# Kernel optimization log

Measured on AMD Instinct MI355X. Metric: run time of the kernel, lower is better.

Reference implementation:

```python
import jax, jax.numpy as jnp
import numpy as np

T, H, D = 8192, 2048, 1024

def setup_inputs() -> dict:
    key = jax.random.key(0)
    k1, k2, k3 = jax.random.split(key, 3)
    x_sequence = jax.random.normal(k1, (T, D), dtype=jnp.float32)
    lamda = jax.random.normal(k2, (H,), dtype=jnp.float32) * 0.2
    B = jax.random.normal(k3, (H, D), dtype=jnp.float32) / jnp.sqrt(jnp.float32(D))
    return {"x_sequence": x_sequence, "lamda": lamda, "B": B}

def reference(x_sequence, lamda, B):
    # Batch all input projections into one GEMM: u[t] = B @ x[t]  -> [T, H]
    u = jnp.einsum('td,hd->th', x_sequence, B)
    a = jax.nn.sigmoid(lamda)  # [H], time-invariant diagonal decay

    def step(h, u_t):
        h = a * h + u_t
        return h, h

    h0 = jnp.zeros_like(lamda)
    _, outputs = jax.lax.scan(step, h0, u)  # [T, H]
    return outputs
```

## Files before the change

kernel.cpp:

```cpp
#include <hip/hip_runtime.h>
#include <hip/hip_bf16.h>

#define T_DIM 8192
#define H_DIM 2048
#define D_DIM 1024
#define PAD_R 32
#define MT    160
#define NT    128
#define BK    64
#define USTR  128

typedef __bf16 bf16x8 __attribute__((ext_vector_type(8)));
typedef float floatx4 __attribute__((ext_vector_type(4)));
typedef unsigned short u16;

__device__ __forceinline__ u16 f2bf(float f) {
    __hip_bfloat16 b = __float2bfloat16(f);
    return *reinterpret_cast<u16*>(&b);
}
__device__ __forceinline__ float bf2f(u16 v) {
    return __uint_as_float((unsigned)v << 16);
}

__global__ __launch_bounds__(256) void conv_kernel(const float* __restrict__ x,
                                                   const float* __restrict__ Bm,
                                                   u16* __restrict__ xb,
                                                   u16* __restrict__ bb) {
    const int nPad4 = PAD_R * D_DIM / 4;
    const int nX4   = (T_DIM + PAD_R) * D_DIM / 4;
    const int nB4   = H_DIM * D_DIM / 4;
    int i = blockIdx.x * 256 + threadIdx.x;
    if (i < nX4) {
        ushort4 o;
        if (i < nPad4) {
            o.x = o.y = o.z = o.w = 0;
        } else {
            const float4 v = reinterpret_cast<const float4*>(x)[i - nPad4];
            o.x = f2bf(v.x); o.y = f2bf(v.y); o.z = f2bf(v.z); o.w = f2bf(v.w);
        }
        reinterpret_cast<ushort4*>(xb)[i] = o;
    } else {
        i -= nX4;
        if (i >= nB4) return;
        const float4 v = reinterpret_cast<const float4*>(Bm)[i];
        ushort4 o;
        o.x = f2bf(v.x); o.y = f2bf(v.y); o.z = f2bf(v.z); o.w = f2bf(v.w);
        reinterpret_cast<ushort4*>(bb)[i] = o;
    }
}

#define GLDS(g, l) \
    __builtin_amdgcn_global_load_lds((const __attribute__((address_space(1))) void*)(g), \
                                     (__attribute__((address_space(3))) void*)(l), 16, 0, 0)

__global__ __launch_bounds__(256) void fused_kernel(const u16* __restrict__ xb,
                                                    const u16* __restrict__ bb,
                                                    const float* __restrict__ lam,
                                                    float* __restrict__ out) {
    __shared__ alignas(16) u16 smem[MT * USTR];
    u16* sA = smem;
    u16* sB = smem + MT * BK;
    u16* us = smem;

    const int tid  = threadIdx.x;
    const int lane = tid & 63;
    const int wid  = tid >> 6;
    const int pm0  = blockIdx.y * 128;
    const int n0   = blockIdx.x * 128;
    const int wm   = (wid >> 1) * 80;
    const int wn   = (wid & 1) * 64;
    const int lrow = lane & 15;
    const int kseg = lane >> 4;

    floatx4 acc[5][4] = {};

    const int r_s = tid >> 3;
    const int cg  = ((tid & 7) * 8) ^ ((r_s & 7) * 8);

    const u16* gA = xb + (size_t)(pm0 + r_s) * D_DIM + cg;
    const u16* gB = bb + (size_t)(n0 + r_s) * D_DIM + cg;

    const bf16x8* pA = reinterpret_cast<const bf16x8*>(sA);
    const bf16x8* pB = reinterpret_cast<const bf16x8*>(sB);

    for (int it = 0; it < D_DIM / BK; ++it) {
#pragma unroll
        for (int q = 0; q < 5; ++q)
            GLDS(gA + (size_t)(q * 32) * D_DIM, &sA[q * 2048 + tid * 8]);
#pragma unroll
        for (int q = 0; q < 4; ++q)
            GLDS(gB + (size_t)(q * 32) * D_DIM, &sB[q * 2048 + tid * 8]);
        gA += BK; gB += BK;
        __syncthreads();

#pragma unroll
        for (int kk = 0; kk < BK; kk += 32) {
            bf16x8 af[5], bf[4];
#pragma unroll
            for (int i = 0; i < 5; ++i) {
                const int row = wm + i * 16 + lrow;
                const int cp  = (kk + kseg * 8) ^ ((row & 7) * 8);
                af[i] = pA[(row * BK + cp) >> 3];
            }
#pragma unroll
            for (int j = 0; j < 4; ++j) {
                const int row = wn + j * 16 + lrow;
                const int cp  = (kk + kseg * 8) ^ ((row & 7) * 8);
                bf[j] = pB[(row * BK + cp) >> 3];
            }
#pragma unroll
            for (int i = 0; i < 5; ++i)
#pragma unroll
                for (int j = 0; j < 4; ++j)
                    acc[i][j] = __builtin_amdgcn_mfma_f32_16x16x32_bf16(af[i], bf[j], acc[i][j], 0, 0, 0);
        }
        __syncthreads();
    }

#pragma unroll
    for (int i = 0; i < 5; ++i) {
#pragma unroll
        for (int j = 0; j < 4; ++j) {
            const int col = wn + j * 16 + lrow;
#pragma unroll
            for (int r = 0; r < 4; ++r) {
                const int row = wm + i * 16 + kseg * 4 + r;
                us[row * USTR + (col ^ (kseg * 16))] = f2bf(acc[i][j][r]);
            }
        }
    }
    __syncthreads();

    {
        const int half = tid >> 7;
        const int c    = tid & 127;
        const float a  = 1.0f / (1.0f + __expf(-lam[n0 + c]));
        float hs = 0.0f;
        const int rbase = half * 64;
        float* op = out + (size_t)(blockIdx.y * 128 + half * 64) * H_DIM + (n0 + c);
#pragma unroll 8
        for (int q = 0; q < 32; ++q) {
            const int tl = rbase + q;
            hs = fmaf(a, hs, bf2f(us[tl * USTR + (c ^ (((tl >> 2) & 3) * 16))]));
        }
#pragma unroll 8
        for (int q = 0; q < 64; ++q) {
            const int tl = rbase + 32 + q;
            hs = fmaf(a, hs, bf2f(us[tl * USTR + (c ^ (((tl >> 2) & 3) * 16))]));
            op[(size_t)q * H_DIM] = hs;
        }
    }
}

extern "C" void kernel_launch(void* const* d_in, const int* in_sizes, int n_in,
                              void* d_out, int out_size, void* d_ws, size_t ws_size,
                              hipStream_t stream) {
    const float* x   = (const float*)d_in[0];
    const float* lam = (const float*)d_in[1];
    const float* B   = (const float*)d_in[2];
    float* out = (float*)d_out;

    u16* xb = (u16*)d_ws;
    u16* bb = xb + (size_t)(T_DIM + PAD_R) * D_DIM;

    const int n4 = ((T_DIM + PAD_R) * D_DIM + H_DIM * D_DIM) / 4;
    conv_kernel<<<(n4 + 255) / 256, 256, 0, stream>>>(x, B, xb, bb);
    fused_kernel<<<dim3(H_DIM / 128, T_DIM / 128), 256, 0, stream>>>(xb, bb, lam, out);
}
```

Baseline: 148.1 us.

## Split fused GEMM+scan into pipelined 256x256 GEMM and separate scan kernel

Replaces the fused GEMM-plus-local-scan kernel, which used 160-row tiles overlapping into previous rows, with a 256x256-tile GEMM. The new GEMM uses 512 threads, double-buffered global-to-LDS loads, barrier-staged MFMA quads with priority hints and XCD-aware block mapping, and writes bf16 u to workspace. A separate scan kernel then rescans with a 32-step warmup and two channels per thread. The aim is to remove the redundant A-tile recompute and raise MFMA efficiency. The cost is an extra bf16 round trip of u through global memory and one more launch.

```diff
diff --git a/kernel.cpp b/kernel.cpp
--- a/kernel.cpp
+++ b/kernel.cpp
@@ -4,11 +4,7 @@
 #define T_DIM 8192
 #define H_DIM 2048
 #define D_DIM 1024
-#define PAD_R 32
-#define MT    160
-#define NT    128
-#define BK    64
-#define USTR  128
+#define KT    16
 
 typedef __bf16 bf16x8 __attribute__((ext_vector_type(8)));
 typedef float floatx4 __attribute__((ext_vector_type(4)));
@@ -21,134 +17,217 @@
 __device__ __forceinline__ float bf2f(u16 v) {
     return __uint_as_float((unsigned)v << 16);
 }
+
+#define GLDS(g, l) \
+    __builtin_amdgcn_global_load_lds((const __attribute__((address_space(1))) void*)(g), \
+                                     (__attribute__((address_space(3))) void*)(l), 16, 0, 0)
 
 __global__ __launch_bounds__(256) void conv_kernel(const float* __restrict__ x,
                                                    const float* __restrict__ Bm,
                                                    u16* __restrict__ xb,
                                                    u16* __restrict__ bb) {
-    const int nPad4 = PAD_R * D_DIM / 4;
-    const int nX4   = (T_DIM + PAD_R) * D_DIM / 4;
-    const int nB4   = H_DIM * D_DIM / 4;
+    const int nX4 = T_DIM * D_DIM / 4;
+    const int nB4 = H_DIM * D_DIM / 4;
     int i = blockIdx.x * 256 + threadIdx.x;
+    const float4* src;
+    ushort4* dst;
     if (i < nX4) {
-        ushort4 o;
-        if (i < nPad4) {
-            o.x = o.y = o.z = o.w = 0;
-        } else {
-            const float4 v = reinterpret_cast<const float4*>(x)[i - nPad4];
-            o.x = f2bf(v.x); o.y = f2bf(v.y); o.z = f2bf(v.z); o.w = f2bf(v.w);
-        }
-        reinterpret_cast<ushort4*>(xb)[i] = o;
+        src = reinterpret_cast<const float4*>(x) + i;
+        dst = reinterpret_cast<ushort4*>(xb) + i;
     } else {
         i -= nX4;
         if (i >= nB4) return;
-        const float4 v = reinterpret_cast<const float4*>(Bm)[i];
-        ushort4 o;
-        o.x = f2bf(v.x); o.y = f2bf(v.y); o.z = f2bf(v.z); o.w = f2bf(v.w);
-        reinterpret_cast<ushort4*>(bb)[i] = o;
-    }
-}
-
-#define GLDS(g, l) \
-    __builtin_amdgcn_global_load_lds((const __attribute__((address_space(1))) void*)(g), \
-                                     (__attribute__((address_space(3))) void*)(l), 16, 0, 0)
-
-__global__ __launch_bounds__(256) void fused_kernel(const u16* __restrict__ xb,
-                                                    const u16* __restrict__ bb,
-                                                    const float* __restrict__ lam,
-                                                    float* __restrict__ out) {
-    __shared__ alignas(16) u16 smem[MT * USTR];
+        src = reinterpret_cast<const float4*>(Bm) + i;
+        dst = reinterpret_cast<ushort4*>(bb) + i;
+    }
+    const float4 v = *src;
+    ushort4 o;
+    o.x = f2bf(v.x); o.y = f2bf(v.y); o.z = f2bf(v.z); o.w = f2bf(v.w);
+    *dst = o;
+}
+
+__device__ __forceinline__ bf16x8 lds_frag(const u16* base, int row, int kx, int kseg) {
+    const int cp = (kx + kseg * 8) ^ ((row & 7) * 8);
+    return *reinterpret_cast<const bf16x8*>(base + row * 64 + cp);
+}
+
+#define MFMA_QUAD(MH, NH, BF)                                                        \
+    _Pragma("unroll")                                                                \
+    for (int kx = 0; kx < 2; ++kx)                                                   \
+        _Pragma("unroll")                                                            \
+        for (int mi = 0; mi < 4; ++mi)                                               \
+            _Pragma("unroll")                                                        \
+            for (int nj = 0; nj < 2; ++nj)                                           \
+                acc[(MH) * 4 + mi][(NH) * 2 + nj] =                                  \
+                    __builtin_amdgcn_mfma_f32_16x16x32_bf16(                         \
+                        af[mi][kx], BF[nj][kx], acc[(MH) * 4 + mi][(NH) * 2 + nj],   \
+                        0, 0, 0);
+
+__global__ __launch_bounds__(512, 2) void gemm_kernel(const u16* __restrict__ xb,
+                                                      const u16* __restrict__ bb,
+                                                      u16* __restrict__ ub) {
+    __shared__ alignas(16) u16 smem[65536];
     u16* sA = smem;
-    u16* sB = smem + MT * BK;
-    u16* us = smem;
+    u16* sB = smem + 32768;
 
     const int tid  = threadIdx.x;
     const int lane = tid & 63;
     const int wid  = tid >> 6;
-    const int pm0  = blockIdx.y * 128;
-    const int n0   = blockIdx.x * 128;
-    const int wm   = (wid >> 1) * 80;
-    const int wn   = (wid & 1) * 64;
     const int lrow = lane & 15;
     const int kseg = lane >> 4;
-
-    floatx4 acc[5][4] = {};
-
-    const int r_s = tid >> 3;
-    const int cg  = ((tid & 7) * 8) ^ ((r_s & 7) * 8);
-
-    const u16* gA = xb + (size_t)(pm0 + r_s) * D_DIM + cg;
-    const u16* gB = bb + (size_t)(n0 + r_s) * D_DIM + cg;
-
-    const bf16x8* pA = reinterpret_cast<const bf16x8*>(sA);
-    const bf16x8* pB = reinterpret_cast<const bf16x8*>(sB);
-
-    for (int it = 0; it < D_DIM / BK; ++it) {
-#pragma unroll
-        for (int q = 0; q < 5; ++q)
-            GLDS(gA + (size_t)(q * 32) * D_DIM, &sA[q * 2048 + tid * 8]);
-#pragma unroll
-        for (int q = 0; q < 4; ++q)
-            GLDS(gB + (size_t)(q * 32) * D_DIM, &sB[q * 2048 + tid * 8]);
-        gA += BK; gB += BK;
-        __syncthreads();
-
-#pragma unroll
-        for (int kk = 0; kk < BK; kk += 32) {
-            bf16x8 af[5], bf[4];
-#pragma unroll
-            for (int i = 0; i < 5; ++i) {
-                const int row = wm + i * 16 + lrow;
-                const int cp  = (kk + kseg * 8) ^ ((row & 7) * 8);
-                af[i] = pA[(row * BK + cp) >> 3];
+    const int wm   = (wid >> 2) * 128;
+    const int wn   = (wid & 3) * 64;
+
+    const int bid = blockIdx.x;
+    const int xcd = bid & 7, idx = bid >> 3;
+    const int bn  = (xcd & 1) * 4 + (idx & 3);
+    const int bm  = (xcd >> 1) * 8 + (idx >> 2);
+
+    const int rS = tid >> 3;
+    const int cS = ((tid & 7) * 8) ^ ((rS & 7) * 8);
+    const u16* gA = xb + (size_t)(bm * 256 + rS) * D_DIM + cS;
+    const u16* gB = bb + (size_t)(bn * 256 + rS) * D_DIM + cS;
+
+    floatx4 acc[8][4] = {};
+    bf16x8 af[4][2], b0[2][2], b1[2][2];
+
+#pragma unroll
+    for (int hq = 0; hq < 4; ++hq)
+        GLDS(gA + (size_t)(hq * 64) * D_DIM, sA + hq * 4096 + tid * 8);
+#pragma unroll
+    for (int hq = 0; hq < 4; ++hq)
+        GLDS(gB + (size_t)(hq * 64) * D_DIM, sB + hq * 4096 + tid * 8);
+#pragma unroll
+    for (int hq = 0; hq < 4; ++hq)
+        GLDS(gB + (size_t)(hq * 64) * D_DIM + 64, sB + 16384 + hq * 4096 + tid * 8);
+    asm volatile("s_waitcnt vmcnt(4)" ::: "memory");
+    __builtin_amdgcn_s_barrier();
+
+#pragma unroll 2
+    for (int j = 0; j < KT; ++j) {
+        const u16* cA = sA + (j & 1) * 16384;
+        const u16* cB = sB + (j & 1) * 16384;
+        u16* dB       = sB + (j & 1) * 16384;
+        const u16* gb2 = gB + (size_t)(j + 2) * 64;
+
+#pragma unroll
+        for (int mi = 0; mi < 4; ++mi)
+#pragma unroll
+            for (int kx = 0; kx < 2; ++kx)
+                af[mi][kx] = lds_frag(cA, wm + mi * 16 + lrow, kx * 32, kseg);
+#pragma unroll
+        for (int nj = 0; nj < 2; ++nj)
+#pragma unroll
+            for (int kx = 0; kx < 2; ++kx)
+                b0[nj][kx] = lds_frag(cB, wn + nj * 16 + lrow, kx * 32, kseg);
+        if (j + 1 < KT) {
+            u16* dA = sA + ((j + 1) & 1) * 16384;
+            const u16* ga = gA + (size_t)(j + 1) * 64;
+#pragma unroll
+            for (int hq = 0; hq < 4; ++hq)
+                GLDS(ga + (size_t)(hq * 64) * D_DIM, dA + hq * 4096 + tid * 8);
+        }
+        __builtin_amdgcn_s_barrier();
+        asm volatile("s_waitcnt lgkmcnt(0)" ::: "memory");
+        __builtin_amdgcn_s_setprio(1);
+        MFMA_QUAD(0, 0, b0)
+        __builtin_amdgcn_s_setprio(0);
+        __builtin_amdgcn_s_barrier();
+
+#pragma unroll
+        for (int nj = 0; nj < 2; ++nj)
+#pragma unroll
+            for (int kx = 0; kx < 2; ++kx)
+                b1[nj][kx] = lds_frag(cB, wn + 32 + nj * 16 + lrow, kx * 32, kseg);
+        __builtin_amdgcn_s_barrier();
+        asm volatile("s_waitcnt lgkmcnt(0)" ::: "memory");
+        __builtin_amdgcn_s_setprio(1);
+        MFMA_QUAD(0, 1, b1)
+        __builtin_amdgcn_s_setprio(0);
+        __builtin_amdgcn_s_barrier();
+
+#pragma unroll
+        for (int mi = 0; mi < 4; ++mi)
+#pragma unroll
+            for (int kx = 0; kx < 2; ++kx)
+                af[mi][kx] = lds_frag(cA, wm + 64 + mi * 16 + lrow, kx * 32, kseg);
+        if (j + 2 < KT) {
+            GLDS(gb2, dB + tid * 8);
+            GLDS(gb2 + (size_t)64 * D_DIM, dB + 4096 + tid * 8);
+        }
+        __builtin_amdgcn_s_barrier();
+        asm volatile("s_waitcnt lgkmcnt(0)" ::: "memory");
+        __builtin_amdgcn_s_setprio(1);
+        MFMA_QUAD(1, 0, b0)
+        __builtin_amdgcn_s_setprio(0);
+        __builtin_amdgcn_s_barrier();
+
+        if (j + 2 < KT) {
+            GLDS(gb2 + (size_t)128 * D_DIM, dB + 8192 + tid * 8);
+            GLDS(gb2 + (size_t)192 * D_DIM, dB + 12288 + tid * 8);
+        }
+        __builtin_amdgcn_s_barrier();
+        asm volatile("s_waitcnt lgkmcnt(0)" ::: "memory");
+        __builtin_amdgcn_s_setprio(1);
+        MFMA_QUAD(1, 1, b1)
+        __builtin_amdgcn_s_setprio(0);
+        if (j < KT - 2) asm volatile("s_waitcnt vmcnt(4)" ::: "memory");
+        else            asm volatile("s_waitcnt vmcnt(0)" ::: "memory");
+        __builtin_amdgcn_s_barrier();
+    }
+
+    u16* ut = smem;
+#pragma unroll
+    for (int mi = 0; mi < 8; ++mi)
+#pragma unroll
+        for (int nj = 0; nj < 4; ++nj) {
+            const int col = wn + nj * 16 + lrow;
+#pragma unroll
+            for (int r = 0; r < 4; ++r) {
+                const int row = wm + mi * 16 + kseg * 4 + r;
+                ut[row * 256 + (col ^ (kseg * 16))] = f2bf(acc[mi][nj][r]);
             }
-#pragma unroll
-            for (int j = 0; j < 4; ++j) {
-                const int row = wn + j * 16 + lrow;
-                const int cp  = (kk + kseg * 8) ^ ((row & 7) * 8);
-                bf[j] = pB[(row * BK + cp) >> 3];
-            }
-#pragma unroll
-            for (int i = 0; i < 5; ++i)
-#pragma unroll
-                for (int j = 0; j < 4; ++j)
-                    acc[i][j] = __builtin_amdgcn_mfma_f32_16x16x32_bf16(af[i], bf[j], acc[i][j], 0, 0, 0);
-        }
-        __syncthreads();
-    }
-
-#pragma unroll
-    for (int i = 0; i < 5; ++i) {
-#pragma unroll
-        for (int j = 0; j < 4; ++j) {
-            const int col = wn + j * 16 + lrow;
-#pragma unroll
-            for (int r = 0; r < 4; ++r) {
-                const int row = wm + i * 16 + kseg * 4 + r;
-                us[row * USTR + (col ^ (kseg * 16))] = f2bf(acc[i][j][r]);
-            }
-        }
-    }
+        }
     __syncthreads();
-
     {
-        const int half = tid >> 7;
-        const int c    = tid & 127;
-        const float a  = 1.0f / (1.0f + __expf(-lam[n0 + c]));
-        float hs = 0.0f;
-        const int rbase = half * 64;
-        float* op = out + (size_t)(blockIdx.y * 128 + half * 64) * H_DIM + (n0 + c);
+        const int rr = tid >> 5, cc = tid & 31;
+#pragma unroll
+        for (int w = 0; w < 16; ++w) {
+            const int row = w * 16 + rr;
+            const int s = (row >> 2) & 3;
+            bf16x8 v = *reinterpret_cast<const bf16x8*>(&ut[row * 256 + ((cc * 8) ^ (s * 16))]);
+            *reinterpret_cast<bf16x8*>(&ub[(size_t)(bm * 256 + row) * H_DIM + bn * 256 + cc * 8]) = v;
+        }
+    }
+}
+
+__global__ __launch_bounds__(256) void scan_kernel(const u16* __restrict__ u,
+                                                   const float* __restrict__ lam,
+                                                   float* __restrict__ out) {
+    const int tid  = threadIdx.x;
+    const int half = tid >> 7;
+    const int c2   = (blockIdx.x * 128 + (tid & 127)) * 2;
+    const int t0   = blockIdx.y * 256 + half * 128;
+    const float a0 = 1.0f / (1.0f + __expf(-lam[c2]));
+    const float a1 = 1.0f / (1.0f + __expf(-lam[c2 + 1]));
+    float h0 = 0.0f, h1 = 0.0f;
+    const u16* up = u + (size_t)t0 * H_DIM + c2;
+    if (t0) {
+        const u16* uw = up - (size_t)32 * H_DIM;
 #pragma unroll 8
         for (int q = 0; q < 32; ++q) {
-            const int tl = rbase + q;
-            hs = fmaf(a, hs, bf2f(us[tl * USTR + (c ^ (((tl >> 2) & 3) * 16))]));
-        }
+            const unsigned v = *reinterpret_cast<const unsigned*>(uw + (size_t)q * H_DIM);
+            h0 = fmaf(a0, h0, bf2f((u16)v));
+            h1 = fmaf(a1, h1, bf2f((u16)(v >> 16)));
+        }
+    }
+    float2* op = reinterpret_cast<float2*>(out + (size_t)t0 * H_DIM + c2);
 #pragma unroll 8
-        for (int q = 0; q < 64; ++q) {
-            const int tl = rbase + 32 + q;
-            hs = fmaf(a, hs, bf2f(us[tl * USTR + (c ^ (((tl >> 2) & 3) * 16))]));
-            op[(size_t)q * H_DIM] = hs;
-        }
+    for (int q = 0; q < 128; ++q) {
+        const unsigned v = *reinterpret_cast<const unsigned*>(up + (size_t)q * H_DIM);
+        h0 = fmaf(a0, h0, bf2f((u16)v));
+        h1 = fmaf(a1, h1, bf2f((u16)(v >> 16)));
+        op[(size_t)q * (H_DIM / 2)] = make_float2(h0, h1);
     }
 }
 
@@ -161,9 +240,11 @@
     float* out = (float*)d_out;
 
     u16* xb = (u16*)d_ws;
-    u16* bb = xb + (size_t)(T_DIM + PAD_R) * D_DIM;
-
-    const int n4 = ((T_DIM + PAD_R) * D_DIM + H_DIM * D_DIM) / 4;
+    u16* bb = xb + (size_t)T_DIM * D_DIM;
+    u16* ub = bb + (size_t)H_DIM * D_DIM;
+
+    const int n4 = (T_DIM * D_DIM + H_DIM * D_DIM) / 4;
     conv_kernel<<<(n4 + 255) / 256, 256, 0, stream>>>(x, B, xb, bb);
-    fused_kernel<<<dim3(H_DIM / 128, T_DIM / 128), 256, 0, stream>>>(xb, bb, lam, out);
-}
+    gemm_kernel<<<256, 512, 0, stream>>>(xb, bb, ub);
+    scan_kernel<<<dim3(H_DIM / 256, T_DIM / 256), 256, 0, stream>>>(ub, lam, out);
+}
```

After: 144.7 us. 1.02x faster.

## Software-pipeline GEMM with double/triple-buffered LDS and XCD-aware block mapping

Applied to the files above, without the earlier changes.

Replaces the single-buffered K loop (BK=64, load-then-sync) with a BK=32 pipeline. A is double-buffered and B triple-buffered, with async global-to-LDS loads issued for future tiles while MFMAs run on the current one, using explicit vmcnt waits and setprio. The grid is flattened and block IDs remapped so each XCD handles a contiguous band of M rows, which should improve L2 reuse. LDS per block shrinks to about 44KB and launch bounds request 3 blocks per CU, trading register headroom for occupancy.

```diff
diff --git a/kernel.cpp b/kernel.cpp
--- a/kernel.cpp
+++ b/kernel.cpp
@@ -5,10 +5,7 @@
 #define H_DIM 2048
 #define D_DIM 1024
 #define PAD_R 32
-#define MT    160
-#define NT    128
-#define BK    64
-#define USTR  128
+#define KT2   32
 
 typedef __bf16 bf16x8 __attribute__((ext_vector_type(8)));
 typedef float floatx4 __attribute__((ext_vector_type(4)));
@@ -21,6 +18,10 @@
 __device__ __forceinline__ float bf2f(u16 v) {
     return __uint_as_float((unsigned)v << 16);
 }
+
+#define GLDS(g, l) \
+    __builtin_amdgcn_global_load_lds((const __attribute__((address_space(1))) void*)(g), \
+                                     (__attribute__((address_space(3))) void*)(l), 16, 0, 0)
 
 __global__ __launch_bounds__(256) void conv_kernel(const float* __restrict__ x,
                                                    const float* __restrict__ Bm,
@@ -49,105 +50,134 @@
     }
 }
 
-#define GLDS(g, l) \
-    __builtin_amdgcn_global_load_lds((const __attribute__((address_space(1))) void*)(g), \
-                                     (__attribute__((address_space(3))) void*)(l), 16, 0, 0)
+__device__ __forceinline__ bf16x8 lds_frag32(const u16* base, int row, int kseg) {
+    const int g = (kseg ^ ((row >> 1) & 3)) * 8;
+    return *reinterpret_cast<const bf16x8*>(base + row * 32 + g);
+}
 
-__global__ __launch_bounds__(256) void fused_kernel(const u16* __restrict__ xb,
-                                                    const u16* __restrict__ bb,
-                                                    const float* __restrict__ lam,
-                                                    float* __restrict__ out) {
-    __shared__ alignas(16) u16 smem[MT * USTR];
+#define PH_BAR()    __builtin_amdgcn_s_barrier()
+#define SCHEDB()    __builtin_amdgcn_sched_barrier(0)
+#define LGKM0()     do { asm volatile("s_waitcnt lgkmcnt(0)" ::: "memory"); \
+                         SCHEDB(); } while (0)
+
+__global__ __launch_bounds__(256, 3) void gemm_kernel(const u16* __restrict__ xb,
+                                                      const u16* __restrict__ bb,
+                                                      const float* __restrict__ lam,
+                                                      float* __restrict__ out) {
+    __shared__ alignas(16) u16 smem[22528];
     u16* sA = smem;
-    u16* sB = smem + MT * BK;
-    u16* us = smem;
+    u16* sB = smem + 10240;
 
     const int tid  = threadIdx.x;
     const int lane = tid & 63;
     const int wid  = tid >> 6;
-    const int pm0  = blockIdx.y * 128;
-    const int n0   = blockIdx.x * 128;
+    const int lrow = lane & 15;
+    const int kseg = lane >> 4;
     const int wm   = (wid >> 1) * 80;
     const int wn   = (wid & 1) * 64;
-    const int lrow = lane & 15;
-    const int kseg = lane >> 4;
+
+    const int bid = blockIdx.x;
+    const int xcd = bid & 7, idx = bid >> 3;
+    const int bn  = idx & 15;
+    const int bm  = xcd * 8 + (idx >> 4);
+
+    const int rS = tid >> 2;
+    const int cS = (((tid & 3) ^ ((tid >> 3) & 3)) * 8);
+    const u16* gA = xb + (size_t)(bm * 128 + rS) * D_DIM + cS;
+    const u16* gB = bb + (size_t)(bn * 128 + rS) * D_DIM + cS;
 
     floatx4 acc[5][4] = {};
+    bf16x8 af[5], bf[4];
 
-    const int r_s = tid >> 3;
-    const int cg  = ((tid & 7) * 8) ^ ((r_s & 7) * 8);
+    GLDS(gA, sA + tid * 8);
+    GLDS(gA + (size_t)64 * D_DIM, sA + 2048 + tid * 8);
+    if (tid < 128)
+        GLDS(gA + (size_t)128 * D_DIM, sA + 4096 + tid * 8);
+    GLDS(gB, sB + tid * 8);
+    GLDS(gB + (size_t)64 * D_DIM, sB + 2048 + tid * 8);
+    GLDS(gB + 32, sB + 4096 + tid * 8);
+    GLDS(gB + (size_t)64 * D_DIM + 32, sB + 6144 + tid * 8);
+    asm volatile("s_waitcnt vmcnt(2)" ::: "memory");
+    PH_BAR();
 
-    const u16* gA = xb + (size_t)(pm0 + r_s) * D_DIM + cg;
-    const u16* gB = bb + (size_t)(n0 + r_s) * D_DIM + cg;
-
-    const bf16x8* pA = reinterpret_cast<const bf16x8*>(sA);
-    const bf16x8* pB = reinterpret_cast<const bf16x8*>(sB);
-
-    for (int it = 0; it < D_DIM / BK; ++it) {
-#pragma unroll
-        for (int q = 0; q < 5; ++q)
-            GLDS(gA + (size_t)(q * 32) * D_DIM, &sA[q * 2048 + tid * 8]);
-#pragma unroll
-        for (int q = 0; q < 4; ++q)
-            GLDS(gB + (size_t)(q * 32) * D_DIM, &sB[q * 2048 + tid * 8]);
-        gA += BK; gB += BK;
-        __syncthreads();
+    int bc = 0;
+#pragma unroll 2
+    for (int t = 0; t < KT2; ++t) {
+        const u16* cA = sA + (t & 1) * 5120;
+        const u16* cB = sB + bc * 4096;
+        u16* wA       = sA + ((t + 1) & 1) * 5120;
+        const int b2  = (bc == 0) ? 2 : bc - 1;
+        u16* wB       = sB + b2 * 4096;
 
 #pragma unroll
-        for (int kk = 0; kk < BK; kk += 32) {
-            bf16x8 af[5], bf[4];
+        for (int mi = 0; mi < 5; ++mi)
+            af[mi] = lds_frag32(cA, wm + mi * 16 + lrow, kseg);
 #pragma unroll
-            for (int i = 0; i < 5; ++i) {
-                const int row = wm + i * 16 + lrow;
-                const int cp  = (kk + kseg * 8) ^ ((row & 7) * 8);
-                af[i] = pA[(row * BK + cp) >> 3];
-            }
+        for (int nj = 0; nj < 4; ++nj)
+            bf[nj] = lds_frag32(cB, wn + nj * 16 + lrow, kseg);
+        SCHEDB();
+
+        if (t + 1 < KT2) {
+            const u16* ga1 = gA + (size_t)(t + 1) * 32;
+            GLDS(ga1, wA + tid * 8);
+            GLDS(ga1 + (size_t)64 * D_DIM, wA + 2048 + tid * 8);
+            if (tid < 128)
+                GLDS(ga1 + (size_t)128 * D_DIM, wA + 4096 + tid * 8);
+        }
+        if (t + 2 < KT2) {
+            const u16* gb2 = gB + (size_t)(t + 2) * 32;
+            GLDS(gb2, wB + tid * 8);
+            GLDS(gb2 + (size_t)64 * D_DIM, wB + 2048 + tid * 8);
+        }
+
+        LGKM0();
+        __builtin_amdgcn_s_setprio(1);
 #pragma unroll
-            for (int j = 0; j < 4; ++j) {
-                const int row = wn + j * 16 + lrow;
-                const int cp  = (kk + kseg * 8) ^ ((row & 7) * 8);
-                bf[j] = pB[(row * BK + cp) >> 3];
-            }
+        for (int mi = 0; mi < 5; ++mi)
 #pragma unroll
-            for (int i = 0; i < 5; ++i)
-#pragma unroll
-                for (int j = 0; j < 4; ++j)
-                    acc[i][j] = __builtin_amdgcn_mfma_f32_16x16x32_bf16(af[i], bf[j], acc[i][j], 0, 0, 0);
-        }
-        __syncthreads();
+            for (int nj = 0; nj < 4; ++nj)
+                acc[mi][nj] = __builtin_amdgcn_mfma_f32_16x16x32_bf16(
+                    af[mi], bf[nj], acc[mi][nj], 0, 0, 0);
+        __builtin_amdgcn_s_setprio(0);
+
+        if (t < KT2 - 2) asm volatile("s_waitcnt vmcnt(2)" ::: "memory");
+        else             asm volatile("s_waitcnt vmcnt(0)" ::: "memory");
+        PH_BAR();
+
+        bc = (bc == 2) ? 0 : bc + 1;
     }
 
+    u16* ut = smem;
 #pragma unroll
-    for (int i = 0; i < 5; ++i) {
+    for (int mi = 0; mi < 5; ++mi)
 #pragma unroll
-        for (int j = 0; j < 4; ++j) {
-            const int col = wn + j * 16 + lrow;
+        for (int nj = 0; nj < 4; ++nj) {
+            const int col = wn + nj * 16 + lrow;
 #pragma unroll
             for (int r = 0; r < 4; ++r) {
-                const int row = wm + i * 16 + kseg * 4 + r;
-                us[row * USTR + (col ^ (kseg * 16))] = f2bf(acc[i][j][r]);
+                const int row = wm + mi * 16 + kseg * 4 + r;
+                ut[row * 128 + (col ^ (kseg * 16))] = f2bf(acc[mi][nj][r]);
             }
         }
-    }
     __syncthreads();
 
     {
         const int half = tid >> 7;
         const int c    = tid & 127;
-        const float a  = 1.0f / (1.0f + __expf(-lam[n0 + c]));
-        float hs = 0.0f;
-        const int rbase = half * 64;
-        float* op = out + (size_t)(blockIdx.y * 128 + half * 64) * H_DIM + (n0 + c);
+        const float a  = 1.0f / (1.0f + __expf(-lam[bn * 128 + c]));
+        const int rb = half * 64;
+        float h = 0.0f;
 #pragma unroll 8
         for (int q = 0; q < 32; ++q) {
-            const int tl = rbase + q;
-            hs = fmaf(a, hs, bf2f(us[tl * USTR + (c ^ (((tl >> 2) & 3) * 16))]));
+            const int l = rb + q;
+            h = fmaf(a, h, bf2f(ut[l * 128 + (c ^ (((l >> 2) & 3) * 16))]));
         }
+        float* op = out + (size_t)(bm * 128 + rb) * H_DIM + bn * 128 + c;
 #pragma unroll 8
         for (int q = 0; q < 64; ++q) {
-            const int tl = rbase + 32 + q;
-            hs = fmaf(a, hs, bf2f(us[tl * USTR + (c ^ (((tl >> 2) & 3) * 16))]));
-            op[(size_t)q * H_DIM] = hs;
+            const int l = rb + 32 + q;
+            h = fmaf(a, h, bf2f(ut[l * 128 + (c ^ (((l >> 2) & 3) * 16))]));
+            op[(size_t)q * H_DIM] = h;
         }
     }
 }
@@ -165,5 +195,5 @@
 
     const int n4 = ((T_DIM + PAD_R) * D_DIM + H_DIM * D_DIM) / 4;
     conv_kernel<<<(n4 + 255) / 256, 256, 0, stream>>>(x, B, xb, bb);
-    fused_kernel<<<dim3(H_DIM / 128, T_DIM / 128), 256, 0, stream>>>(xb, bb, lam, out);
+    gemm_kernel<<<(H_DIM / 128) * (T_DIM / 128), 256, 0, stream>>>(xb, bb, lam, out);
 }
```

Measured after the change: 143.5 us. -3.2%, faster.
